# Performance work log

Measured on AMD Instinct MI355X. Metric: run time of the kernel, lower is better.

## Reference

```python
import jax, jax.numpy as jnp
import numpy as np

N = 50000      # n_nodes
E = 800000     # n_edges
IN_NF = 64     # in_node_nf
HID = 128      # hidden_nf
OUT_NF = 64    # out_node_nf
L = 4          # n_layers
EH = HID // 2  # edge MLP hidden width (edge_nf_ratio=2)
C = 1.0        # aggregation scaling constant


def _w(k, shape):
    # fan-in scaled init (matches nn.Linear scale roughly)
    return jax.random.normal(k, shape, dtype=jnp.float32) / np.sqrt(shape[-2]).astype(np.float32)


def setup_inputs() -> dict:
    key = jax.random.key(0)
    ks = jax.random.split(key, 10)
    h = jax.random.normal(ks[0], (N, IN_NF), dtype=jnp.float32)
    edges = jax.random.randint(ks[1], (2, E), 0, N, dtype=jnp.int32)
    return {
        "h": h,
        "edges": edges,
        "W_in": _w(ks[2], (IN_NF, HID)),
        "b_in": jnp.zeros((HID,), jnp.float32),
        # stacked per-layer GCL params, leading dim L
        "eW1": _w(ks[3], (L, 2 * HID, EH)),
        "eb1": jnp.zeros((L, EH), jnp.float32),
        "eW2": _w(ks[4], (L, EH, EH)),
        "eb2": jnp.zeros((L, EH), jnp.float32),
        "nW1": _w(ks[5], (L, HID + EH, HID)),
        "nb1": jnp.zeros((L, HID), jnp.float32),
        "nW2": _w(ks[6], (L, HID, HID)),
        "nb2": jnp.zeros((L, HID), jnp.float32),
        "W_out": _w(ks[7], (HID, OUT_NF)),
        "b_out": jnp.zeros((OUT_NF,), jnp.float32),
    }


def reference(h, edges, W_in, b_in, eW1, eb1, eW2, eb2, nW1, nb1, nW2, nb2, W_out, b_out):
    row, col = edges[0], edges[1]
    h = h @ W_in + b_in  # [N, HID] embedding_in

    def layer(hc, p):
        w1, b1, w2, b2, m1, c1, m2, c2 = p
        # edge model: gather endpoints, concat, 2-layer SiLU MLP
        m = jnp.concatenate([hc[row], hc[col]], axis=1)          # [E, 2*HID]
        m = jax.nn.silu(m @ w1 + b1)                             # [E, EH]
        m = jax.nn.silu(m @ w2 + b2)                             # [E, EH]
        # node model: scatter-sum messages to source nodes, scale by C
        agg = jax.ops.segment_sum(m, row, num_segments=N) * C    # [N, EH]
        z = jnp.concatenate([hc, agg], axis=1)                   # [N, HID+EH]
        z = jax.nn.silu(z @ m1 + c1)
        z = z @ m2 + c2                                          # [N, HID]
        return hc + z, None  # residual=True

    h, _ = jax.lax.scan(layer, h, (eW1, eb1, eW2, eb2, nW1, nb1, nW2, nb2))
    return h @ W_out + b_out  # [N, OUT_NF] embedding_out
```

## Files before the change

### kernel.cpp

```cpp
#include <hip/hip_runtime.h>
#include <hip/hip_bf16.h>
#include <hip/hip_fp16.h>
#include <cstdint>
#include <cstddef>

#define N_NODES 50000
#define N_EDGES 800000
#define NR      50048
#define NBKT    196
#define BSH     8
#define BCHUNK  2048
#define CAP     6144

typedef __attribute__((ext_vector_type(8))) short short8;
typedef __attribute__((ext_vector_type(4))) float floatx4;
typedef __attribute__((ext_vector_type(2))) float floatx2;
typedef __attribute__((ext_vector_type(4))) unsigned int uintx4;
typedef __attribute__((ext_vector_type(8))) _Float16 half8v;

__device__ inline float bf2f(unsigned short u) {
    union { unsigned int i; float f; } v; v.i = ((unsigned int)u) << 16; return v.f;
}
__device__ inline unsigned short f2bf(float f) {
    union { float f; unsigned int i; } v; v.f = f;
    unsigned int u = v.i;
    return (unsigned short)((u + 0x7FFFu + ((u >> 16) & 1u)) >> 16);
}
__device__ inline unsigned int f2bf_pk(float a, float b) {
    __hip_bfloat162 h2 = __float22bfloat162_rn(make_float2(a, b));
    return *reinterpret_cast<unsigned int*>(&h2);
}
__device__ inline float2 bf2f2(unsigned int u) {
    union { unsigned int i; float f; } lo, hi;
    lo.i = u << 16;
    hi.i = u & 0xFFFF0000u;
    return make_float2(lo.f, hi.f);
}
__device__ inline unsigned short f2fh(float f) {
    _Float16 h = (_Float16)f;
    return __builtin_bit_cast(unsigned short, h);
}
__device__ inline unsigned int f2fh_pk(float a, float b) {
    typedef __attribute__((ext_vector_type(2))) __fp16 h2v;
    h2v r = __builtin_amdgcn_cvt_pkrtz(a, b);
    return __builtin_bit_cast(unsigned int, r);
}
__device__ inline __half2 u2h(unsigned int u) { return __builtin_bit_cast(__half2, u); }
__device__ inline unsigned int h2u(__half2 h) { return __builtin_bit_cast(unsigned int, h); }
__device__ inline __half2 silu_h2(__half2 x) {
    const __half2 nlog2e = __float2half2_rn(-1.4426950408889634f);
    const __half2 one    = __float2half2_rn(1.0f);
    __half2 e = h2exp2(__hmul2(x, nlog2e));
    return __hmul2(x, h2rcp(__hadd2(e, one)));
}
__device__ inline float silu_f(float x) {
    float e = __expf(-x);
    return x * __builtin_amdgcn_rcpf(1.0f + e);
}

__device__ inline int block_excl_scan_256(int v, int* buf) {
    int tid = threadIdx.x;
    buf[tid] = v;
    __syncthreads();
    #pragma unroll
    for (int off = 1; off < 256; off <<= 1) {
        int t = (tid >= off) ? buf[tid - off] : 0;
        __syncthreads();
        buf[tid] += t;
        __syncthreads();
    }
    return buf[tid] - v;
}

__device__ inline void pack_std(const float* __restrict__ src,
                                unsigned short* __restrict__ dst,
                                int NOUT, long j) {
    int i = (int)(j & 7);
    long rest = j >> 3;
    int n = (int)(rest % NOUT);
    int kb = (int)(rest / NOUT);
    dst[j] = f2bf(src[(long)(kb * 8 + i) * NOUT + n]);
}
__device__ inline void pack_std_h(const float* __restrict__ src,
                                  unsigned short* __restrict__ dst,
                                  int NOUT, long j) {
    int i = (int)(j & 7);
    long rest = j >> 3;
    int n = (int)(rest % NOUT);
    int kb = (int)(rest / NOUT);
    dst[j] = f2fh(src[(long)(kb * 8 + i) * NOUT + n]);
}

#define NH0   (N_NODES * 64L)
#define SW_IN 8192L
#define SW_OUT 8192L
#define SW1   16384L
#define SE2   4096L
#define SN1   24576L
#define SN2   16384L
#define SB    128L
#define PERL  (SW1 + SE2 + SN1 + SN2 + SB)
#define PACK_TOTAL (NH0 + SW_IN + SW_OUT + 4 * PERL)

__global__ __launch_bounds__(256) void pack_kernel(
    const float* __restrict__ h0, const float* __restrict__ W_in,
    const float* __restrict__ W_out, const float* __restrict__ eW1,
    const float* __restrict__ eb1, const float* __restrict__ eW2,
    const float* __restrict__ nW1, const float* __restrict__ nW2,
    unsigned short* __restrict__ h0bf, unsigned short* __restrict__ Winp,
    unsigned short* __restrict__ Woutp, unsigned short* __restrict__ W1p,
    unsigned short* __restrict__ eW2p, unsigned short* __restrict__ nW1p,
    unsigned short* __restrict__ nW2p, float* __restrict__ biasP)
{
    long idx = (long)blockIdx.x * 256 + threadIdx.x;
    if (idx >= PACK_TOTAL) return;
    long j = idx;
    if (j < NH0) { h0bf[j] = f2bf(h0[j]); return; }
    j -= NH0;
    if (j < SW_IN) { pack_std(W_in, Winp, 128, j); return; }
    j -= SW_IN;
    if (j < SW_OUT) { pack_std(W_out, Woutp, 64, j); return; }
    j -= SW_OUT;
    int l = (int)(j / PERL);
    long r = j % PERL;
    if (r < SW1) {
        int i = (int)(r & 7);
        int n = (int)((r >> 3) & 127);
        int kb = (int)(r >> 10);
        int k = kb * 8 + i;
        const float* w = eW1 + (long)l * 256 * 64;
        float v = (n < 64) ? w[(long)k * 64 + n] : w[(long)(128 + k) * 64 + (n - 64)];
        W1p[(long)l * SW1 + r] = f2bf(v);
        return;
    }
    r -= SW1;
    if (r < SE2) { pack_std_h(eW2 + (long)l * 4096, eW2p + (long)l * SE2, 64, r); return; }
    r -= SE2;
    if (r < SN1) { pack_std(nW1 + (long)l * 24576, nW1p + (long)l * SN1, 128, r); return; }
    r -= SN1;
    if (r < SN2) { pack_std(nW2 + (long)l * 16384, nW2p + (long)l * SN2, 128, r); return; }
    r -= SN2;
    biasP[(long)l * 128 + r] = (r < 64) ? eb1[(long)l * 64 + r] : 0.0f;
}

__global__ __launch_bounds__(256) void hist_k(const int* __restrict__ erow,
                                              int* __restrict__ countB, int E) {
    __shared__ int c[NBKT];
    for (int i = threadIdx.x; i < NBKT; i += 256) c[i] = 0;
    __syncthreads();
    int j = blockIdx.x * BCHUNK + threadIdx.x;
    #pragma unroll
    for (int i = 0; i < BCHUNK / 256; i++, j += 256)
        if (j < E) atomicAdd(&c[erow[j] >> BSH], 1);
    __syncthreads();
    for (int i = threadIdx.x; i < NBKT; i += 256)
        if (c[i]) atomicAdd(&countB[i], c[i]);
}

__global__ __launch_bounds__(256) void bucket_scan_k(const int* __restrict__ countB,
                                                     int* __restrict__ bucketBase,
                                                     int* __restrict__ bucketCursor) {
    __shared__ int buf[256];
    int tid = threadIdx.x;
    int v = (tid < NBKT) ? countB[tid] : 0;
    int excl = block_excl_scan_256(v, buf);
    if (tid < NBKT) {
        bucketBase[tid] = excl;
        bucketCursor[tid] = excl;
    }
    if (tid == NBKT - 1) bucketBase[NBKT] = excl + v;
}

__global__ __launch_bounds__(256) void bin_k(
    const int* __restrict__ erow, const int* __restrict__ ecol,
    int* __restrict__ bucketCursor, int2* __restrict__ binned, int E)
{
    __shared__ int2 staged[BCHUNK];
    __shared__ int cnt[NBKT];
    __shared__ int binStart[NBKT];
    __shared__ int gbase[NBKT];
    __shared__ int scanbuf[256];
    const int tid = threadIdx.x;
    const int base = blockIdx.x * BCHUNK;
    const int nloc = min(BCHUNK, E - base);

    for (int i = tid; i < NBKT; i += 256) cnt[i] = 0;
    __syncthreads();

    int2 ed[BCHUNK / 256];
    int  bo[BCHUNK / 256];
    #pragma unroll
    for (int i = 0; i < BCHUNK / 256; i++) {
        int jl = i * 256 + tid;
        if (jl < nloc) {
            int j = base + jl;
            int r = erow[j], c = ecol[j];
            ed[i] = make_int2(r, c);
            int b = r >> BSH;
            int off = atomicAdd(&cnt[b], 1);
            bo[i] = (b << 12) | off;
        } else bo[i] = -1;
    }
    __syncthreads();

    int v = (tid < NBKT) ? cnt[tid] : 0;
    int excl = block_excl_scan_256(v, scanbuf);
    if (tid < NBKT) binStart[tid] = excl;
    if (tid < NBKT && v > 0) gbase[tid] = atomicAdd(&bucketCursor[tid], v);
    __syncthreads();

    #pragma unroll
    for (int i = 0; i < BCHUNK / 256; i++) {
        if (bo[i] >= 0)
            staged[binStart[bo[i] >> 12] + (bo[i] & 0xFFF)] = ed[i];
    }
    __syncthreads();

    for (int j = tid; j < nloc; j += 256) {
        int2 e = staged[j];
        int b = e.x >> BSH;
        binned[gbase[b] + (j - binStart[b])] = e;
    }
}

__global__ __launch_bounds__(256) void sort_k(
    const int2* __restrict__ binned, const int* __restrict__ bucketBase,
    int2* __restrict__ eidx)
{
    __shared__ int2 st[CAP];
    __shared__ int cnt[256];
    __shared__ int cur[256];
    __shared__ int scanbuf[256];
    const int b = blockIdx.x;
    const int tid = threadIdx.x;
    const int s0 = bucketBase[b];
    int n = bucketBase[b + 1] - s0;
    if (n > CAP) n = CAP;

    cnt[tid] = 0;
    __syncthreads();
    for (int j = tid; j < n; j += 256) {
        int2 e = binned[s0 + j];
        st[j] = e;
        atomicAdd(&cnt[e.x & 255], 1);
    }
    __syncthreads();
    int excl = block_excl_scan_256(cnt[tid], scanbuf);
    cur[tid] = excl;
    __syncthreads();
    for (int j = tid; j < n; j += 256) {
        int2 e = st[j];
        int pos = atomicAdd(&cur[e.x & 255], 1);
        eidx[s0 + pos] = e;
    }
}

__global__ __launch_bounds__(256) void edge_fused_k(
    const int2* __restrict__ eidx,
    const unsigned short* __restrict__ P,
    const unsigned short* __restrict__ Bp,
    const float* __restrict__ b2, float* __restrict__ agg, int E)
{
    __shared__ float M2s[64 * 66];
    __shared__ int ridS[64];
    const int tid = threadIdx.x;
    const int wave = tid >> 6;
    const int lane = tid & 63;
    const int lrow = lane & 15;
    const int quad = lane >> 4;
    const int e0 = blockIdx.x * 64;
    const int el = wave * 16 + lrow;
    const int e = e0 + el;

    floatx4 acc[4];
    #pragma unroll
    for (int nt = 0; nt < 4; nt++) {
        float bv = b2[nt * 16 + lrow];
        acc[nt] = (floatx4){bv, bv, bv, bv};
    }

    half8v af0 = {};
    half8v af1 = {};
    if (e < E) {
        int2 rc = eidx[e];
        int rr = rc.x, cc = rc.y;
        if (quad == 0) ridS[el] = rr;
        const uintx4* pt = (const uintx4*)(P + (size_t)rr * 128 + quad * 8);
        const uintx4* pb = (const uintx4*)(P + (size_t)cc * 128 + 64 + quad * 8);
        uintx4 t0 = pt[0], t1 = pt[4];
        uintx4 b0 = pb[0], b1 = pb[4];
        uintx4 O0, O1;
        #pragma unroll
        for (int i = 0; i < 4; i++) {
            O0[i] = h2u(silu_h2(__hadd2(u2h(t0[i]), u2h(b0[i]))));
            O1[i] = h2u(silu_h2(__hadd2(u2h(t1[i]), u2h(b1[i]))));
        }
        af0 = __builtin_bit_cast(half8v, O0);
        af1 = __builtin_bit_cast(half8v, O1);
    } else if (quad == 0) {
        ridS[el] = -1;
    }

    #pragma unroll
    for (int nt = 0; nt < 4; nt++) {
        half8v bf0 = *(const half8v*)(Bp + (size_t)((0 * 4 + quad) * 64 + nt * 16 + lrow) * 8);
        acc[nt] = __builtin_amdgcn_mfma_f32_16x16x32_f16(af0, bf0, acc[nt], 0, 0, 0);
        half8v bf1 = *(const half8v*)(Bp + (size_t)((1 * 4 + quad) * 64 + nt * 16 + lrow) * 8);
        acc[nt] = __builtin_amdgcn_mfma_f32_16x16x32_f16(af1, bf1, acc[nt], 0, 0, 0);
    }

    const int elb = wave * 16 + quad * 4;
    #pragma unroll
    for (int nt = 0; nt < 4; nt++) {
        int n = nt * 16 + lrow;
        float* dst = &M2s[n * 66 + elb];
        floatx2 v01 = {silu_f(acc[nt][0]), silu_f(acc[nt][1])};
        floatx2 v23 = {silu_f(acc[nt][2]), silu_f(acc[nt][3])};
        *(floatx2*)(dst)     = v01;
        *(floatx2*)(dst + 2) = v23;
    }
    __syncthreads();

    {
        int rid0 = ridS[lane];
        bool st = (rid0 >= 0) && (lane == 0 || rid0 != ridS[lane - 1]);
        unsigned long long m = __ballot(st);
        int ns = __popcll(m);
        int nvalid = E - e0; if (nvalid > 64) nvalid = 64;
        const float* Mf = &M2s[lane * 66];
        unsigned long long mm = m;
        for (int k = 0; k < wave && mm; k++) mm &= mm - 1;
        int j = wave;
        while (mm) {
            int a = __builtin_ctzll(mm);
            unsigned long long m2 = mm & (mm - 1);
            int b = m2 ? __builtin_ctzll(m2) : nvalid;
            float s = 0.0f;
            int el2 = a;
            if (el2 & 1) { s += Mf[el2]; el2++; }
            for (; el2 + 1 < b; el2 += 2) {
                floatx2 v = *(const floatx2*)(Mf + el2);
                s += v[0] + v[1];
            }
            if (el2 < b) s += Mf[el2];
            int rv = ridS[a];
            if (j == 0 || j == ns - 1)
                atomicAdd(&agg[(size_t)rv * 64 + lane], s);
            else
                agg[(size_t)rv * 64 + lane] = s;
            mm = m2;
            for (int k = 0; k < 3 && mm; k++) mm &= mm - 1;
            j += 4;
        }
    }
}

#define SROW 264
template<int FINAL>
__global__ __launch_bounds__(512) void node_fused_k(
    const unsigned short* __restrict__ hbf, const float* __restrict__ agg,
    const unsigned short* __restrict__ W1, const float* __restrict__ b1,
    const unsigned short* __restrict__ W2, const float* __restrict__ b2,
    const unsigned short* __restrict__ B3, const float* __restrict__ bias3,
    float* __restrict__ hFT, unsigned short* __restrict__ hB,
    unsigned short* __restrict__ Pout, float* __restrict__ outF,
    float* __restrict__ aggZ, int M)
{
    __shared__ unsigned short S[64 * SROW];
    const int tid = threadIdx.x;
    const int m0 = blockIdx.x * 64;
    const int wave = tid >> 6;
    const int lane = tid & 63;
    const int lrow = lane & 15;
    const int quad = lane >> 4;
    const int g = wave >> 1;
    const int h = wave & 1;
    const int row0 = m0 + g * 16 + quad * 4;
    const int elb = g * 16 + quad * 4;

    short8 afa0, afa1;
    {
        const float* ap = agg + (size_t)(m0 + g * 16 + lrow) * 64;
        floatx4 q0 = *(const floatx4*)(ap + quad * 8);
        floatx4 q1 = *(const floatx4*)(ap + quad * 8 + 4);
        floatx4 q2 = *(const floatx4*)(ap + 32 + quad * 8);
        floatx4 q3 = *(const floatx4*)(ap + 32 + quad * 8 + 4);
        unsigned int c0[4] = { f2bf_pk(q0[0], q0[1]), f2bf_pk(q0[2], q0[3]),
                               f2bf_pk(q1[0], q1[1]), f2bf_pk(q1[2], q1[3]) };
        unsigned int c1[4] = { f2bf_pk(q2[0], q2[1]), f2bf_pk(q2[2], q2[3]),
                               f2bf_pk(q3[0], q3[1]), f2bf_pk(q3[2], q3[3]) };
        afa0 = *(const short8*)c0;
        afa1 = *(const short8*)c1;
    }

    floatx4 res4[4];
    #pragma unroll
    for (int j = 0; j < 4; j++) {
        int n = (4 * h + j) * 16 + lrow;
        res4[j] = *(const floatx4*)(hFT + (size_t)n * NR + row0);
    }

    for (int t = tid; t < 64 * 16; t += 512) {
        int rr = t >> 4, c = t & 15;
        int row = m0 + rr;
        uintx4 val = {0, 0, 0, 0};
        if (row < M) val = *(const uintx4*)(hbf + (size_t)row * 128 + c * 8);
        *(uintx4*)(&S[rr * SROW + c * 8]) = val;
    }
    __syncthreads();

    if (!FINAL) {
        floatx4 z = {0, 0, 0, 0};
        for (int t = tid; t < 64 * 16; t += 512) {
            int rr = t >> 4, c = t & 15;
            int row = m0 + rr;
            if (row < M) *(floatx4*)(aggZ + (size_t)row * 64 + c * 4) = z;
        }
    }

    const unsigned short* arow = &S[(g * 16 + lrow) * SROW];

    floatx4 acc[4];
    #pragma unroll
    for (int i = 0; i < 4; i++) acc[i] = (floatx4){0, 0, 0, 0};
    #pragma unroll
    for (int kt = 0; kt < 4; kt++) {
        short8 afrag = *(const short8*)(arow + kt * 32 + quad * 8);
        int kb = kt * 4 + quad;
        #pragma unroll
        for (int j = 0; j < 4; j++) {
            int n = (4 * h + j) * 16 + lrow;
            short8 bfrag = *(const short8*)(W1 + (size_t)(kb * 128 + n) * 8);
            acc[j] = __builtin_amdgcn_mfma_f32_16x16x32_bf16(afrag, bfrag, acc[j], 0, 0, 0);
        }
    }
    #pragma unroll
    for (int j = 0; j < 4; j++) {
        int n = (4 * h + j) * 16 + lrow;
        short8 b4 = *(const short8*)(W1 + (size_t)((16 + quad) * 128 + n) * 8);
        acc[j] = __builtin_amdgcn_mfma_f32_16x16x32_bf16(afa0, b4, acc[j], 0, 0, 0);
        short8 b5 = *(const short8*)(W1 + (size_t)((20 + quad) * 128 + n) * 8);
        acc[j] = __builtin_amdgcn_mfma_f32_16x16x32_bf16(afa1, b5, acc[j], 0, 0, 0);
    }

    #pragma unroll
    for (int j = 0; j < 4; j++) {
        int n = (4 * h + j) * 16 + lrow;
        float bv = b1[n];
        unsigned int p01 = f2bf_pk(silu_f(acc[j][0] + bv), silu_f(acc[j][1] + bv));
        unsigned int p23 = f2bf_pk(silu_f(acc[j][2] + bv), silu_f(acc[j][3] + bv));
        S[(elb + 0) * SROW + 128 + n] = (unsigned short)(p01 & 0xFFFF);
        S[(elb + 1) * SROW + 128 + n] = (unsigned short)(p01 >> 16);
        S[(elb + 2) * SROW + 128 + n] = (unsigned short)(p23 & 0xFFFF);
        S[(elb + 3) * SROW + 128 + n] = (unsigned short)(p23 >> 16);
    }
    __syncthreads();

    floatx4 acc2[4];
    #pragma unroll
    for (int i = 0; i < 4; i++) acc2[i] = (floatx4){0, 0, 0, 0};
    #pragma unroll
    for (int kt = 0; kt < 4; kt++) {
        short8 afrag = *(const short8*)(arow + 128 + kt * 32 + quad * 8);
        int kb = kt * 4 + quad;
        #pragma unroll
        for (int j = 0; j < 4; j++) {
            int n = (4 * h + j) * 16 + lrow;
            short8 bfrag = *(const short8*)(W2 + (size_t)(kb * 128 + n) * 8);
            acc2[j] = __builtin_amdgcn_mfma_f32_16x16x32_bf16(afrag, bfrag, acc2[j], 0, 0, 0);
        }
    }

    #pragma unroll
    for (int j = 0; j < 4; j++) {
        int n = (4 * h + j) * 16 + lrow;
        float bv = b2[n];
        floatx4 v4;
        #pragma unroll
        for (int r = 0; r < 4; r++) v4[r] = acc2[j][r] + bv + res4[j][r];
        unsigned int p01 = f2bf_pk(v4[0], v4[1]);
        unsigned int p23 = f2bf_pk(v4[2], v4[3]);
        S[(elb + 0) * SROW + n] = (unsigned short)(p01 & 0xFFFF);
        S[(elb + 1) * SROW + n] = (unsigned short)(p01 >> 16);
        S[(elb + 2) * SROW + n] = (unsigned short)(p23 & 0xFFFF);
        S[(elb + 3) * SROW + n] = (unsigned short)(p23 >> 16);
        if (!FINAL && row0 < M)
            *(floatx4*)(hFT + (size_t)n * NR + row0) = v4;
    }
    __syncthreads();

    constexpr int NT3 = FINAL ? 2 : 4;
    constexpr int NO3 = FINAL ? 64 : 128;
    floatx4 acc3[NT3];
    #pragma unroll
    for (int i = 0; i < NT3; i++) acc3[i] = (floatx4){0, 0, 0, 0};
    #pragma unroll
    for (int kt = 0; kt < 4; kt++) {
        short8 afrag = *(const short8*)(arow + kt * 32 + quad * 8);
        int kb = kt * 4 + quad;
        #pragma unroll
        for (int j = 0; j < NT3; j++) {
            int n = (NT3 * h + j) * 16 + lrow;
            short8 bfrag = *(const short8*)(B3 + (size_t)(kb * NO3 + n) * 8);
            acc3[j] = __builtin_amdgcn_mfma_f32_16x16x32_bf16(afrag, bfrag, acc3[j], 0, 0, 0);
        }
    }
    #pragma unroll
    for (int j = 0; j < NT3; j++) {
        int n = (NT3 * h + j) * 16 + lrow;
        float bv = bias3[n];
        if (FINAL) {
            #pragma unroll
            for (int r = 0; r < 4; r++)
                ((float*)(&S[(elb + r) * SROW + 128]))[n] = acc3[j][r] + bv;
        } else {
            unsigned int p01 = f2fh_pk(acc3[j][0] + bv, acc3[j][1] + bv);
            unsigned int p23 = f2fh_pk(acc3[j][2] + bv, acc3[j][3] + bv);
            S[(elb + 0) * SROW + 128 + n] = (unsigned short)(p01 & 0xFFFF);
            S[(elb + 1) * SROW + 128 + n] = (unsigned short)(p01 >> 16);
            S[(elb + 2) * SROW + 128 + n] = (unsigned short)(p23 & 0xFFFF);
            S[(elb + 3) * SROW + 128 + n] = (unsigned short)(p23 >> 16);
        }
    }
    __syncthreads();

    if (FINAL) {
        for (int t = tid; t < 64 * 16; t += 512) {
            int rr = t >> 4, c = t & 15;
            int row = m0 + rr;
            if (row < M)
                *(floatx4*)(outF + (size_t)row * 64 + c * 4) =
                    *(const floatx4*)((const float*)(&S[rr * SROW + 128]) + c * 4);
        }
    } else {
        for (int t = tid; t < 64 * 32; t += 512) {
            int rr = t >> 5, c = t & 31;
            int row = m0 + rr;
            if (row < M) {
                if (c < 16)
                    *(uintx4*)(hB + (size_t)row * 128 + c * 8) =
                        *(const uintx4*)(&S[rr * SROW + c * 8]);
                else
                    *(uintx4*)(Pout + (size_t)row * 128 + (c - 16) * 8) =
                        *(const uintx4*)(&S[rr * SROW + 128 + (c - 16) * 8]);
            }
        }
    }
}

#define SROWE 264
__global__ __launch_bounds__(256) void embed_fused_k(
    const unsigned short* __restrict__ h0bf, const unsigned short* __restrict__ Win,
    const float* __restrict__ b_in, const unsigned short* __restrict__ W1,
    const float* __restrict__ biasP, float* __restrict__ hFT,
    unsigned short* __restrict__ hB, unsigned short* __restrict__ Pout, int M)
{
    __shared__ unsigned short S[64 * SROWE];
    const int tid = threadIdx.x;
    const int m0 = blockIdx.x * 64;
    const int wave = tid >> 6;
    const int lane = tid & 63;
    const int lrow = lane & 15;
    const int quad = lane >> 4;
    const int row0 = m0 + wave * 16 + quad * 4;
    const int elb = wave * 16 + quad * 4;

    for (int t = tid; t < 64 * 8; t += 256) {
        int rr = t >> 3, c = t & 7;
        int row = m0 + rr;
        uintx4 val = {0, 0, 0, 0};
        if (row < M) val = *(const uintx4*)(h0bf + (size_t)row * 64 + c * 8);
        *(uintx4*)(&S[rr * SROWE + c * 8]) = val;
    }
    __syncthreads();

    const unsigned short* arow = &S[(wave * 16 + lrow) * SROWE];

    floatx4 acc[8];
    #pragma unroll
    for (int i = 0; i < 8; i++) acc[i] = (floatx4){0, 0, 0, 0};
    #pragma unroll
    for (int kt = 0; kt < 2; kt++) {
        short8 afrag = *(const short8*)(arow + kt * 32 + quad * 8);
        int kb = kt * 4 + quad;
        #pragma unroll
        for (int nt = 0; nt < 8; nt++) {
            short8 bfrag = *(const short8*)(Win + (size_t)(kb * 128 + nt * 16 + lrow) * 8);
            acc[nt] = __builtin_amdgcn_mfma_f32_16x16x32_bf16(afrag, bfrag, acc[nt], 0, 0, 0);
        }
    }

    #pragma unroll
    for (int nt = 0; nt < 8; nt++) {
        int n = nt * 16 + lrow;
        float bv = b_in[n];
        floatx4 v4;
        #pragma unroll
        for (int r = 0; r < 4; r++) v4[r] = acc[nt][r] + bv;
        unsigned int p01 = f2bf_pk(v4[0], v4[1]);
        unsigned int p23 = f2bf_pk(v4[2], v4[3]);
        S[(elb + 0) * SROWE + n] = (unsigned short)(p01 & 0xFFFF);
        S[(elb + 1) * SROWE + n] = (unsigned short)(p01 >> 16);
        S[(elb + 2) * SROWE + n] = (unsigned short)(p23 & 0xFFFF);
        S[(elb + 3) * SROWE + n] = (unsigned short)(p23 >> 16);
        if (row0 < M)
            *(floatx4*)(hFT + (size_t)n * NR + row0) = v4;
    }

    floatx4 acc3[8];
    #pragma unroll
    for (int i = 0; i < 8; i++) acc3[i] = (floatx4){0, 0, 0, 0};
    #pragma unroll
    for (int kt = 0; kt < 4; kt++) {
        short8 afrag = *(const short8*)(arow + kt * 32 + quad * 8);
        int kb = kt * 4 + quad;
        #pragma unroll
        for (int nt = 0; nt < 8; nt++) {
            short8 bfrag = *(const short8*)(W1 + (size_t)(kb * 128 + nt * 16 + lrow) * 8);
            acc3[nt] = __builtin_amdgcn_mfma_f32_16x16x32_bf16(afrag, bfrag, acc3[nt], 0, 0, 0);
        }
    }
    #pragma unroll
    for (int nt = 0; nt < 8; nt++) {
        int n = nt * 16 + lrow;
        float bv = biasP[n];
        unsigned int p01 = f2fh_pk(acc3[nt][0] + bv, acc3[nt][1] + bv);
        unsigned int p23 = f2fh_pk(acc3[nt][2] + bv, acc3[nt][3] + bv);
        S[(elb + 0) * SROWE + 128 + n] = (unsigned short)(p01 & 0xFFFF);
        S[(elb + 1) * SROWE + 128 + n] = (unsigned short)(p01 >> 16);
        S[(elb + 2) * SROWE + 128 + n] = (unsigned short)(p23 & 0xFFFF);
        S[(elb + 3) * SROWE + 128 + n] = (unsigned short)(p23 >> 16);
    }
    __syncthreads();

    for (int t = tid; t < 64 * 32; t += 256) {
        int rr = t / 32, c = t % 32;
        int row = m0 + rr;
        if (row < M) {
            if (c < 16)
                *(uintx4*)(hB + (size_t)row * 128 + c * 8) =
                    *(const uintx4*)(&S[rr * SROWE + c * 8]);
            else
                *(uintx4*)(Pout + (size_t)row * 128 + (c - 16) * 8) =
                    *(const uintx4*)(&S[rr * SROWE + 128 + (c - 16) * 8]);
        }
    }
}

extern "C" void kernel_launch(void* const* d_in, const int* in_sizes, int n_in,
                              void* d_out, int out_size, void* d_ws, size_t ws_size,
                              hipStream_t stream) {
    const float* h0   = (const float*)d_in[0];
    const int*   edges= (const int*)d_in[1];
    const float* W_in = (const float*)d_in[2];
    const float* b_in = (const float*)d_in[3];
    const float* eW1  = (const float*)d_in[4];
    const float* eb1  = (const float*)d_in[5];
    const float* eW2  = (const float*)d_in[6];
    const float* eb2  = (const float*)d_in[7];
    const float* nW1  = (const float*)d_in[8];
    const float* nb1  = (const float*)d_in[9];
    const float* nW2  = (const float*)d_in[10];
    const float* nb2  = (const float*)d_in[11];
    const float* W_out= (const float*)d_in[12];
    const float* b_out= (const float*)d_in[13];
    float* out = (float*)d_out;

    const int E = in_sizes[1] / 2;
    const int* erow = edges;
    const int* ecol = edges + E;

    char* ws = (char*)d_ws;
    unsigned short* hbf  = (unsigned short*)(ws + 0);
    float*          hFT  = (float*)(ws + 12800000);
    unsigned short* P    = (unsigned short*)(ws + 38424576);
    float*          agg  = (float*)(ws + 51224576);
    int2*           binned=(int2*)(ws + 51224576);
    unsigned short* h0bf = (unsigned short*)(ws + 76824576);
    int2*           eidx = (int2*)(ws + 76824576);
    float*          biasP= (float*)(ws + 83224576);
    unsigned short* Winp = (unsigned short*)(ws + 83226624);
    unsigned short* Woutp= (unsigned short*)(ws + 83243008);
    unsigned short* W1p  = (unsigned short*)(ws + 83259392);
    unsigned short* eW2p = (unsigned short*)(ws + 83390464);
    unsigned short* nW1p = (unsigned short*)(ws + 83423232);
    unsigned short* nW2p = (unsigned short*)(ws + 83619840);
    int*            countB=(int*)(ws + 83750912);
    int*            bucketBase=(int*)(ws + 83751936);
    int*            bucketCursor=(int*)(ws + 83752960);

    const int gemm_grid = (N_NODES + 63) / 64;
    const int edge_grid = (E + 63) / 64;
    const int pack_grid = (int)((PACK_TOTAL + 255) / 256);
    const int bin_grid  = (E + BCHUNK - 1) / BCHUNK;

    hipMemsetAsync(countB, 0, NBKT * 4, stream);
    pack_kernel<<<pack_grid, 256, 0, stream>>>(h0, W_in, W_out, eW1, eb1, eW2,
                                               nW1, nW2, h0bf, Winp, Woutp, W1p,
                                               eW2p, nW1p, nW2p, biasP);

    hist_k<<<bin_grid, 256, 0, stream>>>(erow, countB, E);
    bucket_scan_k<<<1, 256, 0, stream>>>(countB, bucketBase, bucketCursor);
    bin_k<<<bin_grid, 256, 0, stream>>>(erow, ecol, bucketCursor, binned, E);

    embed_fused_k<<<gemm_grid, 256, 0, stream>>>(
        h0bf, Winp, b_in, W1p, biasP, hFT, hbf, P, N_NODES);

    sort_k<<<NBKT, 256, 0, stream>>>(binned, bucketBase, eidx);

    hipMemsetAsync(agg, 0, (size_t)N_NODES * 64 * 4, stream);

    for (int l = 0; l < 4; l++) {
        edge_fused_k<<<edge_grid, 256, 0, stream>>>(
            eidx, P, eW2p + (size_t)l * SE2, eb2 + (size_t)l * 64, agg, E);
        if (l < 3) {
            node_fused_k<0><<<gemm_grid, 512, 0, stream>>>(
                hbf, agg, nW1p + (size_t)l * SN1, nb1 + (size_t)l * 128,
                nW2p + (size_t)l * SN2, nb2 + (size_t)l * 128,
                W1p + (size_t)(l + 1) * SW1, biasP + (size_t)(l + 1) * 128,
                hFT, hbf, P, nullptr, agg, N_NODES);
        } else {
            node_fused_k<1><<<gemm_grid, 512, 0, stream>>>(
                hbf, agg, nW1p + (size_t)l * SN1, nb1 + (size_t)l * 128,
                nW2p + (size_t)l * SN2, nb2 + (size_t)l * 128,
                Woutp, b_out, hFT, hbf, nullptr, out, nullptr, N_NODES);
        }
    }
}
```

Before: 439.6 us.

## Process four edge tiles per block with register weights and gather prefetch

The fused edge kernel now handles four consecutive 64-edge groups per block instead of one, and the edge grid shrinks to match. The second-layer MFMA weight fragments and bias are loaded into registers once per block rather than once per tile. The endpoint gathers for the next group are issued before the current group's MFMA and segmented reduction, so gather latency can overlap with compute. The cost is higher register pressure, an extra block barrier per group, and four times fewer blocks to spread across the GPU.

```diff
diff --git a/kernel.cpp b/kernel.cpp
--- a/kernel.cpp
+++ b/kernel.cpp
@@ -11,6 +11,7 @@
 #define BSH     8
 #define BCHUNK  2048
 #define CAP     6144
+#define EGRP    4
 
 typedef __attribute__((ext_vector_type(8))) short short8;
 typedef __attribute__((ext_vector_type(4))) float floatx4;
@@ -268,90 +269,118 @@
     const int lane = tid & 63;
     const int lrow = lane & 15;
     const int quad = lane >> 4;
-    const int e0 = blockIdx.x * 64;
+    const int e0 = blockIdx.x * (64 * EGRP);
     const int el = wave * 16 + lrow;
-    const int e = e0 + el;
-
-    floatx4 acc[4];
-    #pragma unroll
-    for (int nt = 0; nt < 4; nt++) {
-        float bv = b2[nt * 16 + lrow];
-        acc[nt] = (floatx4){bv, bv, bv, bv};
-    }
-
-    half8v af0 = {};
-    half8v af1 = {};
-    if (e < E) {
-        int2 rc = eidx[e];
-        int rr = rc.x, cc = rc.y;
-        if (quad == 0) ridS[el] = rr;
+    const int elb = wave * 16 + quad * 4;
+
+    half8v bfr[8];
+    #pragma unroll
+    for (int kb = 0; kb < 2; kb++)
+        #pragma unroll
+        for (int nt = 0; nt < 4; nt++)
+            bfr[kb * 4 + nt] =
+                *(const half8v*)(Bp + (size_t)((kb * 4 + quad) * 64 + nt * 16 + lrow) * 8);
+    float bias[4];
+    #pragma unroll
+    for (int nt = 0; nt < 4; nt++) bias[nt] = b2[nt * 16 + lrow];
+
+    int2 rc[EGRP];
+    #pragma unroll
+    for (int g = 0; g < EGRP; g++) {
+        int ee = e0 + g * 64 + el;
+        rc[g] = (ee < E) ? eidx[ee] : make_int2(-1, 0);
+    }
+
+    uintx4 t0, t1, b0, b1;
+    {
+        int rr = rc[0].x < 0 ? 0 : rc[0].x;
+        int cc = rc[0].y;
         const uintx4* pt = (const uintx4*)(P + (size_t)rr * 128 + quad * 8);
         const uintx4* pb = (const uintx4*)(P + (size_t)cc * 128 + 64 + quad * 8);
-        uintx4 t0 = pt[0], t1 = pt[4];
-        uintx4 b0 = pb[0], b1 = pb[4];
+        t0 = pt[0]; t1 = pt[4]; b0 = pb[0]; b1 = pb[4];
+    }
+
+    #pragma unroll
+    for (int g = 0; g < EGRP; g++) {
+        int nvalid = E - (e0 + g * 64);
+        if (nvalid <= 0) break;
+        if (nvalid > 64) nvalid = 64;
+
+        if (quad == 0) ridS[el] = rc[g].x;
+
         uintx4 O0, O1;
         #pragma unroll
         for (int i = 0; i < 4; i++) {
             O0[i] = h2u(silu_h2(__hadd2(u2h(t0[i]), u2h(b0[i]))));
             O1[i] = h2u(silu_h2(__hadd2(u2h(t1[i]), u2h(b1[i]))));
         }
-        af0 = __builtin_bit_cast(half8v, O0);
-        af1 = __builtin_bit_cast(half8v, O1);
-    } else if (quad == 0) {
-        ridS[el] = -1;
-    }
-
-    #pragma unroll
-    for (int nt = 0; nt < 4; nt++) {
-        half8v bf0 = *(const half8v*)(Bp + (size_t)((0 * 4 + quad) * 64 + nt * 16 + lrow) * 8);
-        acc[nt] = __builtin_amdgcn_mfma_f32_16x16x32_f16(af0, bf0, acc[nt], 0, 0, 0);
-        half8v bf1 = *(const half8v*)(Bp + (size_t)((1 * 4 + quad) * 64 + nt * 16 + lrow) * 8);
-        acc[nt] = __builtin_amdgcn_mfma_f32_16x16x32_f16(af1, bf1, acc[nt], 0, 0, 0);
-    }
-
-    const int elb = wave * 16 + quad * 4;
-    #pragma unroll
-    for (int nt = 0; nt < 4; nt++) {
-        int n = nt * 16 + lrow;
-        float* dst = &M2s[n * 66 + elb];
-        floatx2 v01 = {silu_f(acc[nt][0]), silu_f(acc[nt][1])};
-        floatx2 v23 = {silu_f(acc[nt][2]), silu_f(acc[nt][3])};
-        *(floatx2*)(dst)     = v01;
-        *(floatx2*)(dst + 2) = v23;
-    }
-    __syncthreads();
-
-    {
-        int rid0 = ridS[lane];
-        bool st = (rid0 >= 0) && (lane == 0 || rid0 != ridS[lane - 1]);
-        unsigned long long m = __ballot(st);
-        int ns = __popcll(m);
-        int nvalid = E - e0; if (nvalid > 64) nvalid = 64;
-        const float* Mf = &M2s[lane * 66];
-        unsigned long long mm = m;
-        for (int k = 0; k < wave && mm; k++) mm &= mm - 1;
-        int j = wave;
-        while (mm) {
-            int a = __builtin_ctzll(mm);
-            unsigned long long m2 = mm & (mm - 1);
-            int b = m2 ? __builtin_ctzll(m2) : nvalid;
-            float s = 0.0f;
-            int el2 = a;
-            if (el2 & 1) { s += Mf[el2]; el2++; }
-            for (; el2 + 1 < b; el2 += 2) {
-                floatx2 v = *(const floatx2*)(Mf + el2);
-                s += v[0] + v[1];
+        half8v af0 = __builtin_bit_cast(half8v, O0);
+        half8v af1 = __builtin_bit_cast(half8v, O1);
+
+        uintx4 nt0, nt1, nb0, nb1;
+        if (g + 1 < EGRP) {
+            int rr = rc[g + 1].x < 0 ? 0 : rc[g + 1].x;
+            int cc = rc[g + 1].y;
+            const uintx4* pt = (const uintx4*)(P + (size_t)rr * 128 + quad * 8);
+            const uintx4* pb = (const uintx4*)(P + (size_t)cc * 128 + 64 + quad * 8);
+            nt0 = pt[0]; nt1 = pt[4]; nb0 = pb[0]; nb1 = pb[4];
+        }
+
+        floatx4 acc[4];
+        #pragma unroll
+        for (int nt = 0; nt < 4; nt++)
+            acc[nt] = (floatx4){bias[nt], bias[nt], bias[nt], bias[nt]};
+        #pragma unroll
+        for (int nt = 0; nt < 4; nt++) {
+            acc[nt] = __builtin_amdgcn_mfma_f32_16x16x32_f16(af0, bfr[nt], acc[nt], 0, 0, 0);
+            acc[nt] = __builtin_amdgcn_mfma_f32_16x16x32_f16(af1, bfr[4 + nt], acc[nt], 0, 0, 0);
+        }
+
+        #pragma unroll
+        for (int nt = 0; nt < 4; nt++) {
+            int n = nt * 16 + lrow;
+            float* dst = &M2s[n * 66 + elb];
+            floatx2 v01 = {silu_f(acc[nt][0]), silu_f(acc[nt][1])};
+            floatx2 v23 = {silu_f(acc[nt][2]), silu_f(acc[nt][3])};
+            *(floatx2*)(dst)     = v01;
+            *(floatx2*)(dst + 2) = v23;
+        }
+        __syncthreads();
+
+        {
+            int rid0 = ridS[lane];
+            bool st = (rid0 >= 0) && (lane == 0 || rid0 != ridS[lane - 1]);
+            unsigned long long m = __ballot(st);
+            int ns = __popcll(m);
+            const float* Mf = &M2s[lane * 66];
+            unsigned long long mm = m;
+            for (int k = 0; k < wave && mm; k++) mm &= mm - 1;
+            int j = wave;
+            while (mm) {
+                int a = __builtin_ctzll(mm);
+                unsigned long long m2 = mm & (mm - 1);
+                int b = m2 ? __builtin_ctzll(m2) : nvalid;
+                float s = 0.0f;
+                int el2 = a;
+                if (el2 & 1) { s += Mf[el2]; el2++; }
+                for (; el2 + 1 < b; el2 += 2) {
+                    floatx2 v = *(const floatx2*)(Mf + el2);
+                    s += v[0] + v[1];
+                }
+                if (el2 < b) s += Mf[el2];
+                int rv = ridS[a];
+                if (j == 0 || j == ns - 1)
+                    atomicAdd(&agg[(size_t)rv * 64 + lane], s);
+                else
+                    agg[(size_t)rv * 64 + lane] = s;
+                mm = m2;
+                for (int k = 0; k < 3 && mm; k++) mm &= mm - 1;
+                j += 4;
             }
-            if (el2 < b) s += Mf[el2];
-            int rv = ridS[a];
-            if (j == 0 || j == ns - 1)
-                atomicAdd(&agg[(size_t)rv * 64 + lane], s);
-            else
-                agg[(size_t)rv * 64 + lane] = s;
-            mm = m2;
-            for (int k = 0; k < 3 && mm; k++) mm &= mm - 1;
-            j += 4;
-        }
+        }
+        __syncthreads();
+
+        if (g + 1 < EGRP) { t0 = nt0; t1 = nt1; b0 = nb0; b1 = nb1; }
     }
 }
 
@@ -690,7 +719,7 @@
     int*            bucketCursor=(int*)(ws + 83752960);
 
     const int gemm_grid = (N_NODES + 63) / 64;
-    const int edge_grid = (E + 63) / 64;
+    const int edge_grid = (E + 64 * EGRP - 1) / (64 * EGRP);
     const int pack_grid = (int)((PACK_TOTAL + 255) / 256);
     const int bin_grid  = (E + BCHUNK - 1) / BCHUNK;
 
```

Result: slower. 467.5 us (+6.3%).
